# Kernel optimization log

Hardware: AMD Instinct MI355X
Metric: run time of the kernel (lower is better)

## Reference

```python
import jax, jax.numpy as jnp
import numpy as np

EPS = 1e-5

def silu(x):
    return x * jax.nn.sigmoid(x)

def layernorm(x, g, b):
    m = jnp.mean(x, axis=-1, keepdims=True)
    v = jnp.var(x, axis=-1, keepdims=True)
    return (x - m) * jax.lax.rsqrt(v + EPS) * g + b

def mamba(x, in_w, conv_w, conv_b, xproj_w, dt_w, dt_b, A_log, Dp, out_w):
    # x: (B, L, d_model)
    B_, L, _ = x.shape
    d_inner, d_conv = conv_w.shape
    d_state = A_log.shape[1]
    dt_rank = dt_w.shape[1]
    xz = x @ in_w.T                     # (B, L, 2*d_inner)
    u, z = jnp.split(xz, 2, axis=-1)
    # causal depthwise conv1d, kernel size d_conv, truncated to L
    up = jnp.pad(u, ((0, 0), (d_conv - 1, 0), (0, 0))).transpose(0, 2, 1)  # (B, C, L+K-1)
    uc = jax.lax.conv_general_dilated(up, conv_w[:, None, :], (1,), 'VALID',
                                      feature_group_count=d_inner)        # (B, C, L)
    u = silu(uc.transpose(0, 2, 1) + conv_b)                               # (B, L, d_inner)
    dbc = u @ xproj_w.T                                                    # (B, L, dt_rank+2*d_state)
    dt, Bm, Cm = jnp.split(dbc, [dt_rank, dt_rank + d_state], axis=-1)
    delta = jax.nn.softplus(dt @ dt_w.T + dt_b)                            # (B, L, d_inner)
    A = -jnp.exp(A_log)                                                    # (d_inner, d_state)
    dA = jnp.exp(delta[..., None] * A)                                     # (B, L, d_inner, d_state)
    dBu = delta[..., None] * Bm[:, :, None, :] * u[..., None]

    def step(h, inp):
        dA_t, dBu_t, C_t = inp
        h = dA_t * h + dBu_t                                               # (B, d_inner, d_state)
        y = jnp.einsum('bdn,bn->bd', h, C_t)
        return h, y

    h0 = jnp.zeros((B_, d_inner, d_state), x.dtype)
    _, ys = jax.lax.scan(step, h0, (dA.transpose(1, 0, 2, 3),
                                    dBu.transpose(1, 0, 2, 3),
                                    Cm.transpose(1, 0, 2)))
    y = ys.transpose(1, 0, 2) + u * Dp
    y = y * silu(z)
    return y @ out_w.T

def decoder_layer(x,
                  f_in_w, f_conv_w, f_conv_b, f_xproj_w, f_dt_w, f_dt_b, f_A_log, f_D, f_out_w,
                  r_in_w, r_conv_w, r_conv_b, r_xproj_w, r_dt_w, r_dt_b, r_A_log, r_D, r_out_w,
                  conv1_w, conv1_b, conv2_w, conv2_b, ln1_g, ln1_b, ln2_g, ln2_b):
    fwd = mamba(x, f_in_w, f_conv_w, f_conv_b, f_xproj_w, f_dt_w, f_dt_b, f_A_log, f_D, f_out_w)
    bwd = jnp.flip(mamba(jnp.flip(x, axis=1), r_in_w, r_conv_w, r_conv_b, r_xproj_w,
                         r_dt_w, r_dt_b, r_A_log, r_D, r_out_w), axis=1)
    x1 = layernorm(x + fwd + bwd, ln1_g, ln1_b)
    # kernel-size-1 Conv1d == pointwise linear; dropout is identity at eval
    y = jax.nn.gelu(x1 @ conv1_w.T + conv1_b, approximate=False)
    y = y @ conv2_w.T + conv2_b
    return layernorm(x1 + y, ln2_g, ln2_b)

def setup_inputs() -> dict:
    key = jax.random.key(0)
    ks = jax.random.split(key, 32)
    d_model, d_state, d_inner, dt_rank, d_ff = 512, 16, 1024, 32, 2048
    B, L = 8, 512
    s = 0.02
    inp = {}
    inp['x'] = jax.random.normal(ks[0], (B, L, d_model), jnp.float32)
    i = 1
    for p in ('f', 'r'):
        inp[p + '_in_w'] = jax.random.normal(ks[i], (2 * d_inner, d_model)) * s; i += 1
        inp[p + '_conv_w'] = jax.random.normal(ks[i], (d_inner, 4)) * 0.2; i += 1
        inp[p + '_conv_b'] = jax.random.normal(ks[i], (d_inner,)) * s; i += 1
        inp[p + '_xproj_w'] = jax.random.normal(ks[i], (dt_rank + 2 * d_state, d_inner)) * s; i += 1
        inp[p + '_dt_w'] = jax.random.normal(ks[i], (d_inner, dt_rank)) * s; i += 1
        inp[p + '_dt_b'] = jax.random.normal(ks[i], (d_inner,)) * s; i += 1
        inp[p + '_A_log'] = jax.random.uniform(ks[i], (d_inner, d_state)); i += 1
        inp[p + '_D'] = jax.random.normal(ks[i], (d_inner,)) * s + 1.0; i += 1
        inp[p + '_out_w'] = jax.random.normal(ks[i], (d_model, d_inner)) * s; i += 1
    inp['conv1_w'] = jax.random.normal(ks[i], (d_ff, d_model)) * s; i += 1
    inp['conv1_b'] = jax.random.normal(ks[i], (d_ff,)) * s; i += 1
    inp['conv2_w'] = jax.random.normal(ks[i], (d_model, d_ff)) * s; i += 1
    inp['conv2_b'] = jax.random.normal(ks[i], (d_model,)) * s; i += 1
    inp['ln1_g'] = jnp.ones((d_model,)); inp['ln1_b'] = jnp.zeros((d_model,))
    inp['ln2_g'] = jnp.ones((d_model,)); inp['ln2_b'] = jnp.zeros((d_model,))
    return inp

def reference(x,
              f_in_w, f_conv_w, f_conv_b, f_xproj_w, f_dt_w, f_dt_b, f_A_log, f_D, f_out_w,
              r_in_w, r_conv_w, r_conv_b, r_xproj_w, r_dt_w, r_dt_b, r_A_log, r_D, r_out_w,
              conv1_w, conv1_b, conv2_w, conv2_b, ln1_g, ln1_b, ln2_g, ln2_b):
    return decoder_layer(x,
                         f_in_w, f_conv_w, f_conv_b, f_xproj_w, f_dt_w, f_dt_b, f_A_log, f_D, f_out_w,
                         r_in_w, r_conv_w, r_conv_b, r_xproj_w, r_dt_w, r_dt_b, r_A_log, r_D, r_out_w,
                         conv1_w, conv1_b, conv2_w, conv2_b, ln1_g, ln1_b, ln2_g, ln2_b)
```

## Files before the change

### kernel.cpp

```cpp
#include <hip/hip_runtime.h>
#include <hip/hip_bf16.h>

#define DEVINL __device__ __forceinline__

typedef short bf16x8 __attribute__((ext_vector_type(8)));
typedef float f32x4 __attribute__((ext_vector_type(4)));
typedef ushort ushort8v __attribute__((ext_vector_type(8)));

static constexpr int Bn = 8, Ln = 512, DM = 512, DI = 1024, DS = 16, DFF = 2048;
static constexpr int Mtok = Bn * Ln;
static constexpr int NCH = 32, CLS = 16;

DEVINL float bf2f(ushort u) { union { uint i; float f; } v; v.i = uint(u) << 16; return v.f; }
DEVINL ushort f2bf(float f) {
  union { float f; uint i; } v; v.f = f;
  uint r = v.i + 0x7FFF + ((v.i >> 16) & 1);
  return ushort(r >> 16);
}

#define GLOAD16(gp, lp)                                                        \
  __builtin_amdgcn_global_load_lds(                                            \
      (const __attribute__((address_space(1))) void*)(gp),                     \
      (__attribute__((address_space(3))) void*)(lp), 16, 0, 0)

struct CvtJob { const float* src; ushort* dst; int blk0; int _pad; };
struct CvtTab { CvtJob j[11]; };

__global__ __launch_bounds__(256)
void cvt_k(CvtTab tb, int njobs) {
  const int blk = blockIdx.x;
  int ji = 0;
#pragma unroll
  for (int k = 1; k < 11; ++k)
    if (k < njobs && tb.j[k].blk0 <= blk) ji = k;
  const CvtJob J = tb.j[ji];
  const size_t base = (size_t)(blk - J.blk0) * 2048 + (size_t)threadIdx.x * 8;
  float4 a = *(const float4*)(J.src + base);
  float4 b = *(const float4*)(J.src + base + 4);
  ushort8v o;
  o[0] = f2bf(a.x); o[1] = f2bf(a.y); o[2] = f2bf(a.z); o[3] = f2bf(a.w);
  o[4] = f2bf(b.x); o[5] = f2bf(b.y); o[6] = f2bf(b.z); o[7] = f2bf(b.w);
  *(ushort8v*)(J.dst + base) = o;
}

template<int BM, int BN, int WM, int WN, int EPI, int OUTF32, int DUALK>
__global__ __launch_bounds__(256)
void gemm_lds(const ushort* __restrict__ A0, const ushort* __restrict__ W0,
              void* __restrict__ C0v, const float* __restrict__ bias0,
              const ushort* __restrict__ A1, const ushort* __restrict__ W1,
              void* __restrict__ C1v, const float* __restrict__ bias1,
              const ushort* __restrict__ Ab0, const ushort* __restrict__ Wb0,
              int K, int lda, int ldw, int ldc, int Kb, int ldab, int ldwb)
{
  constexpr int MT = BM / WM / 16, NT = BN / WN / 16;
  constexpr int RA = BM * 32 / 2048, RB = BN * 32 / 2048;
  __shared__ ushort As[BM * 32];
  __shared__ ushort Bs[BN * 32];

  const ushort* Ap = blockIdx.z ? A1 : A0;
  const ushort* Wp = blockIdx.z ? W1 : W0;
  void* Cv         = blockIdx.z ? C1v : C0v;
  const float* bia = blockIdx.z ? bias1 : bias0;

  const int tid = threadIdx.x, lane = tid & 63, wv = tid >> 6;
  const int wm = wv / WN, wn = wv % WN;
  const int mbase = blockIdx.x * BM, nbase = blockIdx.y * BN;
  const int r = lane & 15, ko = (lane >> 4) * 8;

  f32x4 acc[MT][NT];
#pragma unroll
  for (int mi = 0; mi < MT; ++mi)
#pragma unroll
    for (int ni = 0; ni < NT; ++ni) acc[mi][ni] = (f32x4){0.f, 0.f, 0.f, 0.f};

  for (int blkK = 0; blkK < (DUALK ? 2 : 1); ++blkK) {
    const ushort* Au = (DUALK && blkK) ? Ab0 : Ap;
    const ushort* Wu = (DUALK && blkK) ? Wb0 : Wp;
    const int Ku  = (DUALK && blkK) ? Kb : K;
    const int ldau = (DUALK && blkK) ? ldab : lda;
    const int ldwu = (DUALK && blkK) ? ldwb : ldw;

    for (int k0 = 0; k0 < Ku; k0 += 32) {
      __syncthreads();
#pragma unroll
      for (int i = 0; i < RA; ++i) {
        const int e = i * 2048 + wv * 512 + lane * 8;
        const int row = e >> 5, ck = e & 31;
        GLOAD16(Au + (size_t)(mbase + row) * ldau + k0 + ck,
                (ushort*)As + i * 2048 + wv * 512);
      }
#pragma unroll
      for (int i = 0; i < RB; ++i) {
        const int e = i * 2048 + wv * 512 + lane * 8;
        const int row = e >> 5, ck = e & 31;
        GLOAD16(Wu + (size_t)(nbase + row) * ldwu + k0 + ck,
                (ushort*)Bs + i * 2048 + wv * 512);
      }
      __syncthreads();

      bf16x8 af[MT], bfv[NT];
#pragma unroll
      for (int mi = 0; mi < MT; ++mi)
        af[mi] = *(const bf16x8*)&As[(wm * MT * 16 + mi * 16 + r) * 32 + ko];
#pragma unroll
      for (int ni = 0; ni < NT; ++ni)
        bfv[ni] = *(const bf16x8*)&Bs[(wn * NT * 16 + ni * 16 + r) * 32 + ko];
#pragma unroll
      for (int mi = 0; mi < MT; ++mi)
#pragma unroll
        for (int ni = 0; ni < NT; ++ni)
          acc[mi][ni] = __builtin_amdgcn_mfma_f32_16x16x32_bf16(af[mi], bfv[ni], acc[mi][ni], 0, 0, 0);
    }
  }

  const int rr = (lane >> 4) * 4, cc = lane & 15;
#pragma unroll
  for (int ni = 0; ni < NT; ++ni) {
    const int col = nbase + wn * NT * 16 + ni * 16 + cc;
    float bsv = 0.f;
    if (EPI >= 1) bsv = bia[col];
#pragma unroll
    for (int mi = 0; mi < MT; ++mi) {
#pragma unroll
      for (int j = 0; j < 4; ++j) {
        const int row = mbase + wm * MT * 16 + mi * 16 + rr + j;
        float v = acc[mi][ni][j] + bsv;
        if (EPI == 2) v = (v > 20.f) ? v : __logf(1.f + __expf(v));
        if (EPI == 3) v = 0.5f * v * (1.f + erff(v * 0.70710678f));
        if (OUTF32) ((float*)Cv)[(size_t)row * ldc + col] = v;
        else        ((ushort*)Cv)[(size_t)row * ldc + col] = f2bf(v);
      }
    }
  }
}

template<int WAVES_M, int WAVES_N, int MT, int NT, int EPI, int OUTF32>
__global__ __launch_bounds__(WAVES_M * WAVES_N * 64)
void gemm_k(const ushort* __restrict__ A0, const ushort* __restrict__ W0,
            void* __restrict__ C0v, const float* __restrict__ bias0,
            const ushort* __restrict__ A1, const ushort* __restrict__ W1,
            void* __restrict__ C1v, const float* __restrict__ bias1,
            int K, int lda, int ldw, int ldc)
{
  const ushort* A   = blockIdx.z ? A1 : A0;
  const ushort* W   = blockIdx.z ? W1 : W0;
  void* Cv          = blockIdx.z ? C1v : C0v;
  const float* bia  = blockIdx.z ? bias1 : bias0;

  const int tid = threadIdx.x, lane = tid & 63, wv = tid >> 6;
  const int wm = wv / WAVES_N, wn = wv % WAVES_N;
  const int r = lane & 15, ko = (lane >> 4) * 8;
  const int mbase = blockIdx.x * (WAVES_M * MT * 16) + wm * (MT * 16);
  const int nbase = blockIdx.y * (WAVES_N * NT * 16) + wn * (NT * 16);

  f32x4 acc[MT][NT];
#pragma unroll
  for (int mi = 0; mi < MT; ++mi)
#pragma unroll
    for (int ni = 0; ni < NT; ++ni) acc[mi][ni] = (f32x4){0.f, 0.f, 0.f, 0.f};

  const ushort* arow[MT];
  const ushort* wrow[NT];
#pragma unroll
  for (int mi = 0; mi < MT; ++mi) arow[mi] = A + (size_t)(mbase + mi * 16 + r) * lda + ko;
#pragma unroll
  for (int ni = 0; ni < NT; ++ni) wrow[ni] = W + (size_t)(nbase + ni * 16 + r) * ldw + ko;
  for (int k0 = 0; k0 < K; k0 += 32) {
    bf16x8 av[MT], bv[NT];
#pragma unroll
    for (int mi = 0; mi < MT; ++mi) av[mi] = *(const bf16x8*)(arow[mi] + k0);
#pragma unroll
    for (int ni = 0; ni < NT; ++ni) bv[ni] = *(const bf16x8*)(wrow[ni] + k0);
#pragma unroll
    for (int mi = 0; mi < MT; ++mi)
#pragma unroll
      for (int ni = 0; ni < NT; ++ni)
        acc[mi][ni] = __builtin_amdgcn_mfma_f32_16x16x32_bf16(av[mi], bv[ni], acc[mi][ni], 0, 0, 0);
  }

  const int rr = (lane >> 4) * 4, cc = lane & 15;
#pragma unroll
  for (int ni = 0; ni < NT; ++ni) {
    const int col = nbase + ni * 16 + cc;
    float bsv = 0.f;
    if (EPI >= 1) bsv = bia[col];
#pragma unroll
    for (int mi = 0; mi < MT; ++mi) {
#pragma unroll
      for (int j = 0; j < 4; ++j) {
        const int row = mbase + mi * 16 + rr + j;
        float v = acc[mi][ni][j] + bsv;
        if (EPI == 2) v = (v > 20.f) ? v : __logf(1.f + __expf(v));
        if (OUTF32) ((float*)Cv)[(size_t)row * ldc + col] = v;
        else        ((ushort*)Cv)[(size_t)row * ldc + col] = f2bf(v);
      }
    }
  }
}

__global__ __launch_bounds__(256)
void xproj_k(const ushort* __restrict__ A0, const ushort* __restrict__ W0,
             ushort* __restrict__ C0,
             const ushort* __restrict__ A1, const ushort* __restrict__ W1,
             ushort* __restrict__ C1)
{
  const ushort* A = blockIdx.z ? A1 : A0;
  const ushort* W = blockIdx.z ? W1 : W0;
  ushort* C       = blockIdx.z ? C1 : C0;

  const int tid = threadIdx.x, lane = tid & 63, wv = tid >> 6;
  const int r = lane & 15, ko = (lane >> 4) * 8;
  const int mbase = blockIdx.x * 16;
  const int nbase = wv * 16;

  f32x4 acc = (f32x4){0.f, 0.f, 0.f, 0.f};
  const ushort* ap = A + (size_t)(mbase + r) * DI + ko;
  const ushort* wp = W + (size_t)(nbase + r) * DI + ko;
#pragma unroll 4
  for (int k0 = 0; k0 < DI; k0 += 32) {
    const bf16x8 av = *(const bf16x8*)(ap + k0);
    const bf16x8 bv = *(const bf16x8*)(wp + k0);
    acc = __builtin_amdgcn_mfma_f32_16x16x32_bf16(av, bv, acc, 0, 0, 0);
  }
  const int cc = lane & 15, rr = (lane >> 4) * 4;
#pragma unroll
  for (int j = 0; j < 4; ++j)
    C[(size_t)(mbase + rr + j) * 64 + nbase + cc] = f2bf(acc[j]);
}

__global__ __launch_bounds__(256)
void conv_k(const ushort* __restrict__ xz_f, const ushort* __restrict__ xz_r,
            const float* __restrict__ fw, const float* __restrict__ fb,
            const float* __restrict__ rw, const float* __restrict__ rb,
            ushort* __restrict__ u_f, ushort* __restrict__ u_r,
            ushort* __restrict__ gz_f, ushort* __restrict__ gz_r)
{
  int idx = blockIdx.x * 256 + threadIdx.x;
  int dir = idx >> 19;
  int rem = idx & ((1 << 19) - 1);
  int bt = rem >> 7;
  int c0 = (rem & 127) * 8;
  int b = bt >> 9, t = bt & 511;
  const ushort* xz = dir ? xz_r : xz_f;
  const float* cw = dir ? rw : fw;
  const float* cb = dir ? rb : fb;
  ushort* uo = dir ? u_r : u_f;
  ushort* go = dir ? gz_r : gz_f;

  float acc[8];
#pragma unroll
  for (int j = 0; j < 8; ++j) acc[j] = cb[c0 + j];
  float wgt[8][4];
#pragma unroll
  for (int j = 0; j < 8; ++j) {
    float4 w4 = *(const float4*)(cw + (size_t)(c0 + j) * 4);
    wgt[j][0] = w4.x; wgt[j][1] = w4.y; wgt[j][2] = w4.z; wgt[j][3] = w4.w;
  }
#pragma unroll
  for (int k = 0; k < 4; ++k) {
    int tt = dir ? (t + 3 - k) : (t - 3 + k);
    if (tt < 0 || tt >= Ln) continue;
    ushort8v v = *(const ushort8v*)(xz + ((size_t)(b * Ln + tt) * 2048 + c0));
#pragma unroll
    for (int j = 0; j < 8; ++j) acc[j] += wgt[j][k] * bf2f(v[j]);
  }
  ushort8v outv;
#pragma unroll
  for (int j = 0; j < 8; ++j) {
    float s = acc[j];
    outv[j] = f2bf(s / (1.f + __expf(-s)));
  }
  *(ushort8v*)(uo + (size_t)bt * DI + c0) = outv;

  ushort8v zv = *(const ushort8v*)(xz + ((size_t)bt * 2048 + DI + c0));
  ushort8v gv;
#pragma unroll
  for (int j = 0; j < 8; ++j) {
    float z = bf2f(zv[j]);
    gv[j] = f2bf(z / (1.f + __expf(-z)));
  }
  *(ushort8v*)(go + (size_t)bt * DI + c0) = gv;
}

__global__ __launch_bounds__(256, 4)
void scan1_k(const ushort* __restrict__ delta_f, const ushort* __restrict__ delta_r,
             const ushort* __restrict__ u_f, const ushort* __restrict__ u_r,
             const ushort* __restrict__ dbc_f, const ushort* __restrict__ dbc_r,
             const float* __restrict__ fA, const float* __restrict__ rA,
             float4* __restrict__ hloc, float* __restrict__ Sa)
{
  const int bid = blockIdx.x;
  const int part = bid & 3, chunk = (bid >> 2) & 31, b = (bid >> 7) & 7, dir = bid >> 10;
  const int tid = threadIdx.x, c = part * 256 + tid;
  const int bd = dir * 8 + b;

  const ushort* dl_p = dir ? delta_r : delta_f;
  const ushort* u_p  = dir ? u_r : u_f;
  const ushort* dbc  = dir ? dbc_r : dbc_f;
  const float*  Alog = dir ? rA : fA;

  __shared__ float Bs[CLS][16];
  __shared__ float a2T[16][256];
  {
    const int s = tid >> 4, n = tid & 15;
    const int t = dir ? (Ln - 1 - (chunk * CLS + s)) : (chunk * CLS + s);
    Bs[s][n] = bf2f(dbc[(size_t)(b * Ln + t) * 64 + 32 + n]);
  }
  {
    const float4* Ar = (const float4*)(Alog + (size_t)c * 16);
#pragma unroll
    for (int g = 0; g < 4; ++g) {
      float4 av = Ar[g];
      a2T[g*4+0][tid] = -__expf(av.x) * 1.44269504f;
      a2T[g*4+1][tid] = -__expf(av.y) * 1.44269504f;
      a2T[g*4+2][tid] = -__expf(av.z) * 1.44269504f;
      a2T[g*4+3][tid] = -__expf(av.w) * 1.44269504f;
    }
  }
  __syncthreads();

  const int t0 = dir ? (Ln - 1 - chunk * CLS) : (chunk * CLS);
  const int stp = (dir ? -1 : 1) * DI;
  const ushort* dlp = dl_p + (size_t)(b * Ln + t0) * DI + c;
  const ushort* up  = u_p  + (size_t)(b * Ln + t0) * DI + c;

  float h[16];
#pragma unroll
  for (int n = 0; n < 16; ++n) h[n] = 0.f;
  float S = 0.f;

#pragma unroll 2
  for (int s = 0; s < CLS; ++s) {
    const float dl = bf2f(*dlp); dlp += stp;
    const float uv = bf2f(*up); up += stp;
    const float du = dl * uv;
    S += dl;
#pragma unroll
    for (int g = 0; g < 4; ++g) {
      const float4 Bv = ((const float4*)Bs[s])[g];
      h[g*4+0] = fmaf(exp2f(dl * a2T[g*4+0][tid]), h[g*4+0], du * Bv.x);
      h[g*4+1] = fmaf(exp2f(dl * a2T[g*4+1][tid]), h[g*4+1], du * Bv.y);
      h[g*4+2] = fmaf(exp2f(dl * a2T[g*4+2][tid]), h[g*4+2], du * Bv.z);
      h[g*4+3] = fmaf(exp2f(dl * a2T[g*4+3][tid]), h[g*4+3], du * Bv.w);
    }
  }
#pragma unroll
  for (int g = 0; g < 4; ++g) {
    const size_t o = ((size_t)g * 16 * NCH + (size_t)bd * NCH + chunk) * 1024 + c;
    hloc[o] = (float4){h[g*4+0], h[g*4+1], h[g*4+2], h[g*4+3]};
  }
  Sa[((size_t)bd * NCH + chunk) * 1024 + c] = S;
}

__global__ __launch_bounds__(256, 4)
void scan2_k(float4* __restrict__ hloc, const float* __restrict__ Sa,
             const float* __restrict__ fA, const float* __restrict__ rA)
{
  const int idx = blockIdx.x * 256 + threadIdx.x;
  const int ng = idx & 3, c = (idx >> 2) & 1023, b = (idx >> 12) & 7, dir = idx >> 15;
  const int bd = dir * 8 + b;
  const float* Alog = dir ? rA : fA;
  float a2[4];
  {
    const float4 av = *(const float4*)(Alog + (size_t)c * 16 + ng * 4);
    a2[0] = -__expf(av.x) * 1.44269504f;
    a2[1] = -__expf(av.y) * 1.44269504f;
    a2[2] = -__expf(av.z) * 1.44269504f;
    a2[3] = -__expf(av.w) * 1.44269504f;
  }
  float4 h = (float4){0.f, 0.f, 0.f, 0.f};
#pragma unroll
  for (int k = 0; k < NCH; ++k) {
    const size_t o = ((size_t)ng * 16 * NCH + (size_t)bd * NCH + k) * 1024 + c;
    const float S = Sa[((size_t)bd * NCH + k) * 1024 + c];
    const float4 hl = hloc[o];
    hloc[o] = h;
    h.x = fmaf(exp2f(a2[0] * S), h.x, hl.x);
    h.y = fmaf(exp2f(a2[1] * S), h.y, hl.y);
    h.z = fmaf(exp2f(a2[2] * S), h.z, hl.z);
    h.w = fmaf(exp2f(a2[3] * S), h.w, hl.w);
  }
}

__global__ __launch_bounds__(256, 4)
void scan3_k(const ushort* __restrict__ delta_f, const ushort* __restrict__ delta_r,
             const ushort* __restrict__ u_f, const ushort* __restrict__ u_r,
             const ushort* __restrict__ dbc_f, const ushort* __restrict__ dbc_r,
             const ushort* __restrict__ gz_f, const ushort* __restrict__ gz_r,
             const float* __restrict__ fA, const float* __restrict__ fD,
             const float* __restrict__ rA, const float* __restrict__ rD,
             const float4* __restrict__ hin,
             ushort* __restrict__ ym_f, ushort* __restrict__ ym_r)
{
  const int bid = blockIdx.x;
  const int part = bid & 3, chunk = (bid >> 2) & 31, b = (bid >> 7) & 7, dir = bid >> 10;
  const int tid = threadIdx.x, c = part * 256 + tid;
  const int bd = dir * 8 + b;

  const ushort* dl_p = dir ? delta_r : delta_f;
  const ushort* u_p  = dir ? u_r : u_f;
  const ushort* dbc  = dir ? dbc_r : dbc_f;
  const ushort* gz   = dir ? gz_r : gz_f;
  const float*  Alog = dir ? rA : fA;
  const float*  Dw   = dir ? rD : fD;
  ushort* ym         = dir ? ym_r : ym_f;

  __shared__ float Bs[CLS][16], Cs[CLS][16];
  __shared__ float a2T[16][256];
  {
    const int s = tid >> 5, k = tid & 31;
#pragma unroll
    for (int p = 0; p < 2; ++p) {
      const int ss = s + p * 8;
      const int t = dir ? (Ln - 1 - (chunk * CLS + ss)) : (chunk * CLS + ss);
      const float val = bf2f(dbc[(size_t)(b * Ln + t) * 64 + 32 + k]);
      if (k < 16) Bs[ss][k] = val; else Cs[ss][k - 16] = val;
    }
  }
  {
    const float4* Ar = (const float4*)(Alog + (size_t)c * 16);
#pragma unroll
    for (int g = 0; g < 4; ++g) {
      float4 av = Ar[g];
      a2T[g*4+0][tid] = -__expf(av.x) * 1.44269504f;
      a2T[g*4+1][tid] = -__expf(av.y) * 1.44269504f;
      a2T[g*4+2][tid] = -__expf(av.z) * 1.44269504f;
      a2T[g*4+3][tid] = -__expf(av.w) * 1.44269504f;
    }
  }
  __syncthreads();

  const float Dc = Dw[c];

  float h[16];
#pragma unroll
  for (int g = 0; g < 4; ++g) {
    const size_t o = ((size_t)g * 16 * NCH + (size_t)bd * NCH + chunk) * 1024 + c;
    const float4 hv = hin[o];
    h[g*4+0] = hv.x; h[g*4+1] = hv.y; h[g*4+2] = hv.z; h[g*4+3] = hv.w;
  }

  const int t0 = dir ? (Ln - 1 - chunk * CLS) : (chunk * CLS);
  const int stp = (dir ? -1 : 1) * DI;
  const ushort* dlp = dl_p + (size_t)(b * Ln + t0) * DI + c;
  const ushort* up  = u_p  + (size_t)(b * Ln + t0) * DI + c;
  const ushort* gp  = gz   + (size_t)(b * Ln + t0) * DI + c;
  ushort*       ymp = ym   + (size_t)(b * Ln + t0) * DI + c;

#pragma unroll 2
  for (int s = 0; s < CLS; ++s) {
    const float dl = bf2f(*dlp); dlp += stp;
    const float uv = bf2f(*up); up += stp;
    const float gg = bf2f(*gp); gp += stp;
    const float du = dl * uv;
    float y = 0.f;
#pragma unroll
    for (int g = 0; g < 4; ++g) {
      const float4 Bv = ((const float4*)Bs[s])[g];
      const float4 Cw = ((const float4*)Cs[s])[g];
      h[g*4+0] = fmaf(exp2f(dl * a2T[g*4+0][tid]), h[g*4+0], du * Bv.x); y = fmaf(h[g*4+0], Cw.x, y);
      h[g*4+1] = fmaf(exp2f(dl * a2T[g*4+1][tid]), h[g*4+1], du * Bv.y); y = fmaf(h[g*4+1], Cw.y, y);
      h[g*4+2] = fmaf(exp2f(dl * a2T[g*4+2][tid]), h[g*4+2], du * Bv.z); y = fmaf(h[g*4+2], Cw.z, y);
      h[g*4+3] = fmaf(exp2f(dl * a2T[g*4+3][tid]), h[g*4+3], du * Bv.w); y = fmaf(h[g*4+3], Cw.w, y);
    }
    *ymp = f2bf((y + uv * Dc) * gg); ymp += stp;
  }
}

template<int OUTF32>
__global__ __launch_bounds__(256)
void ln_k(const ushort* __restrict__ a, const ushort* __restrict__ b,
          const float* __restrict__ g, const float* __restrict__ bb,
          void* __restrict__ outv)
{
  const int row = blockIdx.x, tid = threadIdx.x;
  const size_t base = (size_t)row * DM;
  float v0 = bf2f(a[base + tid]) + bf2f(b[base + tid]);
  float v1 = bf2f(a[base + tid + 256]) + bf2f(b[base + tid + 256]);
  float s1 = v0 + v1, s2 = v0 * v0 + v1 * v1;
  for (int o = 32; o; o >>= 1) { s1 += __shfl_down(s1, o); s2 += __shfl_down(s2, o); }
  __shared__ float l1[4], l2[4];
  const int wv = tid >> 6, ln = tid & 63;
  if (ln == 0) { l1[wv] = s1; l2[wv] = s2; }
  __syncthreads();
  const float t1 = l1[0] + l1[1] + l1[2] + l1[3];
  const float t2 = l2[0] + l2[1] + l2[2] + l2[3];
  const float mean = t1 * (1.f / 512.f);
  const float var = t2 * (1.f / 512.f) - mean * mean;
  const float rs = rsqrtf(var + 1e-5f);
  const float o0 = (v0 - mean) * rs * g[tid] + bb[tid];
  const float o1 = (v1 - mean) * rs * g[tid + 256] + bb[tid + 256];
  if (OUTF32) {
    ((float*)outv)[base + tid] = o0;
    ((float*)outv)[base + tid + 256] = o1;
  } else {
    ((ushort*)outv)[base + tid] = f2bf(o0);
    ((ushort*)outv)[base + tid + 256] = f2bf(o1);
  }
}

extern "C" void kernel_launch(void* const* d_in, const int* in_sizes, int n_in,
                              void* d_out, int out_size, void* d_ws, size_t ws_size,
                              hipStream_t stream)
{
  const float* x        = (const float*)d_in[0];
  const float* f_in_w   = (const float*)d_in[1];
  const float* f_conv_w = (const float*)d_in[2];
  const float* f_conv_b = (const float*)d_in[3];
  const float* f_xproj  = (const float*)d_in[4];
  const float* f_dt_w   = (const float*)d_in[5];
  const float* f_dt_b   = (const float*)d_in[6];
  const float* f_A_log  = (const float*)d_in[7];
  const float* f_D      = (const float*)d_in[8];
  const float* f_out_w  = (const float*)d_in[9];
  const float* r_in_w   = (const float*)d_in[10];
  const float* r_conv_w = (const float*)d_in[11];
  const float* r_conv_b = (const float*)d_in[12];
  const float* r_xproj  = (const float*)d_in[13];
  const float* r_dt_w   = (const float*)d_in[14];
  const float* r_dt_b   = (const float*)d_in[15];
  const float* r_A_log  = (const float*)d_in[16];
  const float* r_D      = (const float*)d_in[17];
  const float* r_out_w  = (const float*)d_in[18];
  const float* conv1_w  = (const float*)d_in[19];
  const float* conv1_b  = (const float*)d_in[20];
  const float* conv2_w  = (const float*)d_in[21];
  const float* conv2_b  = (const float*)d_in[22];
  const float* ln1_g    = (const float*)d_in[23];
  const float* ln1_b    = (const float*)d_in[24];
  const float* ln2_g    = (const float*)d_in[25];
  const float* ln2_b    = (const float*)d_in[26];

  char* ws = (char*)d_ws;
  size_t off = 0;
  auto alloc = [&](size_t bytes) -> void* {
    void* p = ws + off;
    off += (bytes + 255) & ~(size_t)255;
    return p;
  };
  ushort* x_b     = (ushort*)alloc((size_t)Mtok * DM * 2);
  ushort* f_inw_b = (ushort*)alloc((size_t)2 * DI * DM * 2);
  ushort* r_inw_b = (ushort*)alloc((size_t)2 * DI * DM * 2);
  ushort* f_xp_b  = (ushort*)alloc((size_t)64 * DI * 2);
  ushort* r_xp_b  = (ushort*)alloc((size_t)64 * DI * 2);
  ushort* f_dtw_b = (ushort*)alloc((size_t)DI * 32 * 2);
  ushort* r_dtw_b = (ushort*)alloc((size_t)DI * 32 * 2);
  ushort* f_ow_b  = (ushort*)alloc((size_t)DM * DI * 2);
  ushort* r_ow_b  = (ushort*)alloc((size_t)DM * DI * 2);
  ushort* c1w_b   = (ushort*)alloc((size_t)DFF * DM * 2);
  ushort* c2w_b   = (ushort*)alloc((size_t)DM * DFF * 2);
  ushort* xz_f    = (ushort*)alloc((size_t)Mtok * 2048 * 2);
  ushort* xz_r    = (ushort*)alloc((size_t)Mtok * 2048 * 2);
  ushort* u_f     = (ushort*)alloc((size_t)Mtok * DI * 2);
  ushort* u_r     = (ushort*)alloc((size_t)Mtok * DI * 2);
  ushort* gz_f    = (ushort*)alloc((size_t)Mtok * DI * 2);
  ushort* gz_r    = (ushort*)alloc((size_t)Mtok * DI * 2);
  ushort* dbc_f   = (ushort*)alloc((size_t)Mtok * 64 * 2);
  ushort* dbc_r   = (ushort*)alloc((size_t)Mtok * 64 * 2);
  ushort* delta_f = (ushort*)alloc((size_t)Mtok * DI * 2);
  ushort* delta_r = (ushort*)alloc((size_t)Mtok * DI * 2);
  ushort* ym_f    = (ushort*)alloc((size_t)Mtok * DI * 2);
  ushort* ym_r    = (ushort*)alloc((size_t)Mtok * DI * 2);
  ushort* mo      = (ushort*)alloc((size_t)Mtok * DM * 2);
  ushort* x1      = (ushort*)alloc((size_t)Mtok * DM * 2);
  ushort* h1b     = (ushort*)alloc((size_t)Mtok * DFF * 2);
  ushort* y2      = (ushort*)alloc((size_t)Mtok * DM * 2);
  float4* hloc    = (float4*)alloc((size_t)4 * 16 * NCH * 1024 * 16);
  float*  Sa      = (float*)alloc((size_t)16 * NCH * 1024 * 4);
  (void)ws_size; (void)in_sizes; (void)n_in; (void)out_size;

  {
    CvtTab tb;
    int blk = 0, ji = 0;
    auto add = [&](const float* s, ushort* d, int n) {
      tb.j[ji].src = s; tb.j[ji].dst = d; tb.j[ji].blk0 = blk; tb.j[ji]._pad = 0;
      blk += n / 2048; ++ji;
    };
    add(x,       x_b,     Mtok * DM);
    add(f_in_w,  f_inw_b, 2 * DI * DM);
    add(r_in_w,  r_inw_b, 2 * DI * DM);
    add(f_xproj, f_xp_b,  64 * DI);
    add(r_xproj, r_xp_b,  64 * DI);
    add(f_dt_w,  f_dtw_b, DI * 32);
    add(r_dt_w,  r_dtw_b, DI * 32);
    add(f_out_w, f_ow_b,  DM * DI);
    add(r_out_w, r_ow_b,  DM * DI);
    add(conv1_w, c1w_b,   DFF * DM);
    add(conv2_w, c2w_b,   DM * DFF);
    cvt_k<<<dim3(blk), 256, 0, stream>>>(tb, ji);
  }

  gemm_lds<128, 128, 2, 2, 0, 0, 0><<<dim3(32, 16, 2), 256, 0, stream>>>(
      x_b, f_inw_b, xz_f, nullptr, x_b, r_inw_b, xz_r, nullptr,
      nullptr, nullptr, DM, DM, DM, 2048, 0, 0, 0);

  conv_k<<<dim3(2 * Mtok * DI / 8 / 256), 256, 0, stream>>>(
      xz_f, xz_r, f_conv_w, f_conv_b, r_conv_w, r_conv_b, u_f, u_r, gz_f, gz_r);

  xproj_k<<<dim3(256, 1, 2), 256, 0, stream>>>(
      u_f, f_xp_b, dbc_f, u_r, r_xp_b, dbc_r);

  gemm_k<4, 1, 1, 4, 2, 0><<<dim3(64, 16, 2), 256, 0, stream>>>(
      dbc_f, f_dtw_b, delta_f, f_dt_b, dbc_r, r_dtw_b, delta_r, r_dt_b,
      32, 64, 32, DI);

  scan1_k<<<dim3(2048), 256, 0, stream>>>(
      delta_f, delta_r, u_f, u_r, dbc_f, dbc_r, f_A_log, r_A_log, hloc, Sa);
  scan2_k<<<dim3(256), 256, 0, stream>>>(hloc, Sa, f_A_log, r_A_log);
  scan3_k<<<dim3(2048), 256, 0, stream>>>(
      delta_f, delta_r, u_f, u_r, dbc_f, dbc_r, gz_f, gz_r,
      f_A_log, f_D, r_A_log, r_D, hloc, ym_f, ym_r);

  gemm_lds<64, 64, 2, 2, 0, 0, 1><<<dim3(64, 8, 1), 256, 0, stream>>>(
      ym_f, f_ow_b, mo, nullptr, nullptr, nullptr, nullptr, nullptr,
      ym_r, r_ow_b, DI, DI, DI, DM, DI, DI, DI);

  ln_k<0><<<dim3(Mtok), 256, 0, stream>>>(x_b, mo, ln1_g, ln1_b, x1);

  gemm_lds<128, 128, 2, 2, 3, 0, 0><<<dim3(32, 16, 1), 256, 0, stream>>>(
      x1, c1w_b, h1b, conv1_b, nullptr, nullptr, nullptr, nullptr,
      nullptr, nullptr, DM, DM, DM, DFF, 0, 0, 0);

  gemm_lds<64, 64, 2, 2, 1, 0, 0><<<dim3(64, 8, 1), 256, 0, stream>>>(
      h1b, c2w_b, y2, conv2_b, nullptr, nullptr, nullptr, nullptr,
      nullptr, nullptr, DFF, DFF, DFF, DM, 0, 0, 0);

  ln_k<1><<<dim3(Mtok), 256, 0, stream>>>(x1, y2, ln2_g, ln2_b, (float*)d_out);
}
```

Baseline: 280.4 us.

## Store delta, u and gate in 16-token blocked layout for vectorized scan loads

```diff
diff --git a/kernel.cpp b/kernel.cpp
--- a/kernel.cpp
+++ b/kernel.cpp
@@ -134,7 +134,7 @@
   }
 }
 
-template<int WAVES_M, int WAVES_N, int MT, int NT, int EPI, int OUTF32>
+template<int WAVES_M, int WAVES_N, int MT, int NT, int EPI, int OUTF32, int BLKOUT>
 __global__ __launch_bounds__(WAVES_M * WAVES_N * 64)
 void gemm_k(const ushort* __restrict__ A0, const ushort* __restrict__ W0,
             void* __restrict__ C0v, const float* __restrict__ bias0,
@@ -191,8 +191,13 @@
         const int row = mbase + mi * 16 + rr + j;
         float v = acc[mi][ni][j] + bsv;
         if (EPI == 2) v = (v > 20.f) ? v : __logf(1.f + __expf(v));
-        if (OUTF32) ((float*)Cv)[(size_t)row * ldc + col] = v;
-        else        ((ushort*)Cv)[(size_t)row * ldc + col] = f2bf(v);
+        if (BLKOUT) {
+          ((ushort*)Cv)[((size_t)(row >> 4) * ldc + col) * 16 + (row & 15)] = f2bf(v);
+        } else if (OUTF32) {
+          ((float*)Cv)[(size_t)row * ldc + col] = v;
+        } else {
+          ((ushort*)Cv)[(size_t)row * ldc + col] = f2bf(v);
+        }
       }
     }
   }
@@ -233,7 +238,8 @@
             const float* __restrict__ fw, const float* __restrict__ fb,
             const float* __restrict__ rw, const float* __restrict__ rb,
             ushort* __restrict__ u_f, ushort* __restrict__ u_r,
-            ushort* __restrict__ gz_f, ushort* __restrict__ gz_r)
+            ushort* __restrict__ ub_f, ushort* __restrict__ ub_r,
+            ushort* __restrict__ gb_f, ushort* __restrict__ gb_r)
 {
   int idx = blockIdx.x * 256 + threadIdx.x;
   int dir = idx >> 19;
@@ -245,7 +251,8 @@
   const float* cw = dir ? rw : fw;
   const float* cb = dir ? rb : fb;
   ushort* uo = dir ? u_r : u_f;
-  ushort* go = dir ? gz_r : gz_f;
+  ushort* ub = dir ? ub_r : ub_f;
+  ushort* gb = dir ? gb_r : gb_f;
 
   float acc[8];
 #pragma unroll
@@ -272,19 +279,37 @@
   }
   *(ushort8v*)(uo + (size_t)bt * DI + c0) = outv;
 
+  const size_t blkb = ((size_t)(bt >> 4) * 1024 + c0) * 16 + (bt & 15);
+#pragma unroll
+  for (int j = 0; j < 8; ++j) ub[blkb + (size_t)j * 16] = outv[j];
+
   ushort8v zv = *(const ushort8v*)(xz + ((size_t)bt * 2048 + DI + c0));
-  ushort8v gv;
 #pragma unroll
   for (int j = 0; j < 8; ++j) {
     float z = bf2f(zv[j]);
-    gv[j] = f2bf(z / (1.f + __expf(-z)));
-  }
-  *(ushort8v*)(go + (size_t)bt * DI + c0) = gv;
-}
+    gb[blkb + (size_t)j * 16] = f2bf(z / (1.f + __expf(-z)));
+  }
+}
+
+#define SCAN1_STEP(s, e)                                                       \
+  {                                                                            \
+    const float dl = bf2f((ushort)(((e) < 8) ? dv0[(e)] : dv1[(e) - 8]));      \
+    const float uv = bf2f((ushort)(((e) < 8) ? uv0[(e)] : uv1[(e) - 8]));      \
+    const float du = dl * uv;                                                  \
+    S += dl;                                                                   \
+    _Pragma("unroll")                                                          \
+    for (int g = 0; g < 4; ++g) {                                              \
+      const float4 Bv = ((const float4*)Bs[(s)])[g];                           \
+      h[g*4+0] = fmaf(exp2f(dl * a2T[g*4+0][tid]), h[g*4+0], du * Bv.x);       \
+      h[g*4+1] = fmaf(exp2f(dl * a2T[g*4+1][tid]), h[g*4+1], du * Bv.y);       \
+      h[g*4+2] = fmaf(exp2f(dl * a2T[g*4+2][tid]), h[g*4+2], du * Bv.z);       \
+      h[g*4+3] = fmaf(exp2f(dl * a2T[g*4+3][tid]), h[g*4+3], du * Bv.w);       \
+    }                                                                          \
+  }
 
 __global__ __launch_bounds__(256, 4)
-void scan1_k(const ushort* __restrict__ delta_f, const ushort* __restrict__ delta_r,
-             const ushort* __restrict__ u_f, const ushort* __restrict__ u_r,
+void scan1_k(const ushort* __restrict__ db_f, const ushort* __restrict__ db_r,
+             const ushort* __restrict__ ub_f, const ushort* __restrict__ ub_r,
              const ushort* __restrict__ dbc_f, const ushort* __restrict__ dbc_r,
              const float* __restrict__ fA, const float* __restrict__ rA,
              float4* __restrict__ hloc, float* __restrict__ Sa)
@@ -294,8 +319,8 @@
   const int tid = threadIdx.x, c = part * 256 + tid;
   const int bd = dir * 8 + b;
 
-  const ushort* dl_p = dir ? delta_r : delta_f;
-  const ushort* u_p  = dir ? u_r : u_f;
+  const ushort* dblk = dir ? db_r : db_f;
+  const ushort* ublk = dir ? ub_r : ub_f;
   const ushort* dbc  = dir ? dbc_r : dbc_f;
   const float*  Alog = dir ? rA : fA;
 
@@ -319,31 +344,26 @@
   }
   __syncthreads();
 
-  const int t0 = dir ? (Ln - 1 - chunk * CLS) : (chunk * CLS);
-  const int stp = (dir ? -1 : 1) * DI;
-  const ushort* dlp = dl_p + (size_t)(b * Ln + t0) * DI + c;
-  const ushort* up  = u_p  + (size_t)(b * Ln + t0) * DI + c;
+  const int sc = dir ? (31 - chunk) : chunk;
+  const size_t blkBase = (((size_t)(b * 32 + sc)) * 1024 + c) * 16;
+  const ushort8v dv0 = *(const ushort8v*)(dblk + blkBase);
+  const ushort8v dv1 = *(const ushort8v*)(dblk + blkBase + 8);
+  const ushort8v uv0 = *(const ushort8v*)(ublk + blkBase);
+  const ushort8v uv1 = *(const ushort8v*)(ublk + blkBase + 8);
 
   float h[16];
 #pragma unroll
   for (int n = 0; n < 16; ++n) h[n] = 0.f;
   float S = 0.f;
 
-#pragma unroll 2
-  for (int s = 0; s < CLS; ++s) {
-    const float dl = bf2f(*dlp); dlp += stp;
-    const float uv = bf2f(*up); up += stp;
-    const float du = dl * uv;
-    S += dl;
-#pragma unroll
-    for (int g = 0; g < 4; ++g) {
-      const float4 Bv = ((const float4*)Bs[s])[g];
-      h[g*4+0] = fmaf(exp2f(dl * a2T[g*4+0][tid]), h[g*4+0], du * Bv.x);
-      h[g*4+1] = fmaf(exp2f(dl * a2T[g*4+1][tid]), h[g*4+1], du * Bv.y);
-      h[g*4+2] = fmaf(exp2f(dl * a2T[g*4+2][tid]), h[g*4+2], du * Bv.z);
-      h[g*4+3] = fmaf(exp2f(dl * a2T[g*4+3][tid]), h[g*4+3], du * Bv.w);
-    }
-  }
+  if (!dir) {
+#pragma unroll
+    for (int s = 0; s < CLS; ++s) SCAN1_STEP(s, s)
+  } else {
+#pragma unroll
+    for (int s = 0; s < CLS; ++s) SCAN1_STEP(s, 15 - s)
+  }
+
 #pragma unroll
   for (int g = 0; g < 4; ++g) {
     const size_t o = ((size_t)g * 16 * NCH + (size_t)bd * NCH + chunk) * 1024 + c;
@@ -382,11 +402,35 @@
   }
 }
 
+#define SCAN3_STEP(s, e)                                                       \
+  {                                                                            \
+    const float dl = bf2f((ushort)(((e) < 8) ? dv0[(e)] : dv1[(e) - 8]));      \
+    const float uv = bf2f((ushort)(((e) < 8) ? uv0[(e)] : uv1[(e) - 8]));      \
+    const float gg = bf2f((ushort)(((e) < 8) ? gv0[(e)] : gv1[(e) - 8]));      \
+    const float du = dl * uv;                                                  \
+    float y = 0.f;                                                             \
+    _Pragma("unroll")                                                          \
+    for (int g = 0; g < 4; ++g) {                                              \
+      const float4 Bv = ((const float4*)Bs[(s)])[g];                           \
+      const float4 Cw = ((const float4*)Cs[(s)])[g];                           \
+      h[g*4+0] = fmaf(exp2f(dl * a2T[g*4+0][tid]), h[g*4+0], du * Bv.x);       \
+      y = fmaf(h[g*4+0], Cw.x, y);                                             \
+      h[g*4+1] = fmaf(exp2f(dl * a2T[g*4+1][tid]), h[g*4+1], du * Bv.y);       \
+      y = fmaf(h[g*4+1], Cw.y, y);                                             \
+      h[g*4+2] = fmaf(exp2f(dl * a2T[g*4+2][tid]), h[g*4+2], du * Bv.z);       \
+      y = fmaf(h[g*4+2], Cw.z, y);                                             \
+      h[g*4+3] = fmaf(exp2f(dl * a2T[g*4+3][tid]), h[g*4+3], du * Bv.w);       \
+      y = fmaf(h[g*4+3], Cw.w, y);                                             \
+    }                                                                          \
+    *ymp = f2bf((y + uv * Dc) * gg);                                           \
+    ymp += stp;                                                                \
+  }
+
 __global__ __launch_bounds__(256, 4)
-void scan3_k(const ushort* __restrict__ delta_f, const ushort* __restrict__ delta_r,
-             const ushort* __restrict__ u_f, const ushort* __restrict__ u_r,
+void scan3_k(const ushort* __restrict__ db_f, const ushort* __restrict__ db_r,
+             const ushort* __restrict__ ub_f, const ushort* __restrict__ ub_r,
              const ushort* __restrict__ dbc_f, const ushort* __restrict__ dbc_r,
-             const ushort* __restrict__ gz_f, const ushort* __restrict__ gz_r,
+             const ushort* __restrict__ gb_f, const ushort* __restrict__ gb_r,
              const float* __restrict__ fA, const float* __restrict__ fD,
              const float* __restrict__ rA, const float* __restrict__ rD,
              const float4* __restrict__ hin,
@@ -397,10 +441,10 @@
   const int tid = threadIdx.x, c = part * 256 + tid;
   const int bd = dir * 8 + b;
 
-  const ushort* dl_p = dir ? delta_r : delta_f;
-  const ushort* u_p  = dir ? u_r : u_f;
+  const ushort* dblk = dir ? db_r : db_f;
+  const ushort* ublk = dir ? ub_r : ub_f;
+  const ushort* gblk = dir ? gb_r : gb_f;
   const ushort* dbc  = dir ? dbc_r : dbc_f;
-  const ushort* gz   = dir ? gz_r : gz_f;
   const float*  Alog = dir ? rA : fA;
   const float*  Dw   = dir ? rD : fD;
   ushort* ym         = dir ? ym_r : ym_f;
@@ -432,6 +476,15 @@
 
   const float Dc = Dw[c];
 
+  const int sc = dir ? (31 - chunk) : chunk;
+  const size_t blkBase = (((size_t)(b * 32 + sc)) * 1024 + c) * 16;
+  const ushort8v dv0 = *(const ushort8v*)(dblk + blkBase);
+  const ushort8v dv1 = *(const ushort8v*)(dblk + blkBase + 8);
+  const ushort8v uv0 = *(const ushort8v*)(ublk + blkBase);
+  const ushort8v uv1 = *(const ushort8v*)(ublk + blkBase + 8);
+  const ushort8v gv0 = *(const ushort8v*)(gblk + blkBase);
+  const ushort8v gv1 = *(const ushort8v*)(gblk + blkBase + 8);
+
   float h[16];
 #pragma unroll
   for (int g = 0; g < 4; ++g) {
@@ -442,28 +495,14 @@
 
   const int t0 = dir ? (Ln - 1 - chunk * CLS) : (chunk * CLS);
   const int stp = (dir ? -1 : 1) * DI;
-  const ushort* dlp = dl_p + (size_t)(b * Ln + t0) * DI + c;
-  const ushort* up  = u_p  + (size_t)(b * Ln + t0) * DI + c;
-  const ushort* gp  = gz   + (size_t)(b * Ln + t0) * DI + c;
-  ushort*       ymp = ym   + (size_t)(b * Ln + t0) * DI + c;
-
-#pragma unroll 2
-  for (int s = 0; s < CLS; ++s) {
-    const float dl = bf2f(*dlp); dlp += stp;
-    const float uv = bf2f(*up); up += stp;
-    const float gg = bf2f(*gp); gp += stp;
-    const float du = dl * uv;
-    float y = 0.f;
-#pragma unroll
-    for (int g = 0; g < 4; ++g) {
-      const float4 Bv = ((const float4*)Bs[s])[g];
-      const float4 Cw = ((const float4*)Cs[s])[g];
-      h[g*4+0] = fmaf(exp2f(dl * a2T[g*4+0][tid]), h[g*4+0], du * Bv.x); y = fmaf(h[g*4+0], Cw.x, y);
-      h[g*4+1] = fmaf(exp2f(dl * a2T[g*4+1][tid]), h[g*4+1], du * Bv.y); y = fmaf(h[g*4+1], Cw.y, y);
-      h[g*4+2] = fmaf(exp2f(dl * a2T[g*4+2][tid]), h[g*4+2], du * Bv.z); y = fmaf(h[g*4+2], Cw.z, y);
-      h[g*4+3] = fmaf(exp2f(dl * a2T[g*4+3][tid]), h[g*4+3], du * Bv.w); y = fmaf(h[g*4+3], Cw.w, y);
-    }
-    *ymp = f2bf((y + uv * Dc) * gg); ymp += stp;
+  ushort* ymp = ym + (size_t)(b * Ln + t0) * DI + c;
+
+  if (!dir) {
+#pragma unroll
+    for (int s = 0; s < CLS; ++s) SCAN3_STEP(s, s)
+  } else {
+#pragma unroll
+    for (int s = 0; s < CLS; ++s) SCAN3_STEP(s, 15 - s)
   }
 }
 
@@ -553,12 +592,14 @@
   ushort* xz_r    = (ushort*)alloc((size_t)Mtok * 2048 * 2);
   ushort* u_f     = (ushort*)alloc((size_t)Mtok * DI * 2);
   ushort* u_r     = (ushort*)alloc((size_t)Mtok * DI * 2);
-  ushort* gz_f    = (ushort*)alloc((size_t)Mtok * DI * 2);
-  ushort* gz_r    = (ushort*)alloc((size_t)Mtok * DI * 2);
+  ushort* ub_f    = (ushort*)alloc((size_t)Mtok * DI * 2);
+  ushort* ub_r    = (ushort*)alloc((size_t)Mtok * DI * 2);
+  ushort* gb_f    = (ushort*)alloc((size_t)Mtok * DI * 2);
+  ushort* gb_r    = (ushort*)alloc((size_t)Mtok * DI * 2);
   ushort* dbc_f   = (ushort*)alloc((size_t)Mtok * 64 * 2);
   ushort* dbc_r   = (ushort*)alloc((size_t)Mtok * 64 * 2);
-  ushort* delta_f = (ushort*)alloc((size_t)Mtok * DI * 2);
-  ushort* delta_r = (ushort*)alloc((size_t)Mtok * DI * 2);
+  ushort* db_f    = (ushort*)alloc((size_t)Mtok * DI * 2);
+  ushort* db_r    = (ushort*)alloc((size_t)Mtok * DI * 2);
   ushort* ym_f    = (ushort*)alloc((size_t)Mtok * DI * 2);
   ushort* ym_r    = (ushort*)alloc((size_t)Mtok * DI * 2);
   ushort* mo      = (ushort*)alloc((size_t)Mtok * DM * 2);
@@ -595,20 +636,21 @@
       nullptr, nullptr, DM, DM, DM, 2048, 0, 0, 0);
 
   conv_k<<<dim3(2 * Mtok * DI / 8 / 256), 256, 0, stream>>>(
-      xz_f, xz_r, f_conv_w, f_conv_b, r_conv_w, r_conv_b, u_f, u_r, gz_f, gz_r);
+      xz_f, xz_r, f_conv_w, f_conv_b, r_conv_w, r_conv_b,
+      u_f, u_r, ub_f, ub_r, gb_f, gb_r);
 
   xproj_k<<<dim3(256, 1, 2), 256, 0, stream>>>(
       u_f, f_xp_b, dbc_f, u_r, r_xp_b, dbc_r);
 
-  gemm_k<4, 1, 1, 4, 2, 0><<<dim3(64, 16, 2), 256, 0, stream>>>(
-      dbc_f, f_dtw_b, delta_f, f_dt_b, dbc_r, r_dtw_b, delta_r, r_dt_b,
+  gemm_k<4, 1, 1, 4, 2, 0, 1><<<dim3(64, 16, 2), 256, 0, stream>>>(
+      dbc_f, f_dtw_b, db_f, f_dt_b, dbc_r, r_dtw_b, db_r, r_dt_b,
       32, 64, 32, DI);
 
   scan1_k<<<dim3(2048), 256, 0, stream>>>(
-      delta_f, delta_r, u_f, u_r, dbc_f, dbc_r, f_A_log, r_A_log, hloc, Sa);
+      db_f, db_r, ub_f, ub_r, dbc_f, dbc_r, f_A_log, r_A_log, hloc, Sa);
   scan2_k<<<dim3(256), 256, 0, stream>>>(hloc, Sa, f_A_log, r_A_log);
   scan3_k<<<dim3(2048), 256, 0, stream>>>(
-      delta_f, delta_r, u_f, u_r, dbc_f, dbc_r, gz_f, gz_r,
+      db_f, db_r, ub_f, ub_r, dbc_f, dbc_r, gb_f, gb_r,
       f_A_log, f_D, r_A_log, r_D, hloc, ym_f, ym_r);
 
   gemm_lds<64, 64, 2, 2, 0, 0, 1><<<dim3(64, 8, 1), 256, 0, stream>>>(
```

After: 345.4 us. 23.2% more time.
